# Kernel optimization log

Hardware: AMD Instinct MI355X
Metric: run time of the kernel (lower is better)

## Reference

```python
import jax, jax.numpy as jnp
import numpy as np

COMMITMENT_COST = 0.25
CODE_BOOK_SIZE = 1024
EMBED_DIM = 64


def setup_inputs() -> dict:
    key = jax.random.key(0)
    k1, k2 = jax.random.split(key)
    inputs = jax.random.normal(k1, (32, 64, 32, 32), dtype=jnp.float32)
    # matches torch init: uniform(-1/K, 1/K)
    embedding = jax.random.uniform(
        k2, (CODE_BOOK_SIZE, EMBED_DIM), dtype=jnp.float32,
        minval=-1.0 / CODE_BOOK_SIZE, maxval=1.0 / CODE_BOOK_SIZE)
    return {"inputs": inputs, "embedding": embedding}


def reference(inputs, embedding):
    # inputs: [B, D, H, W] -> [B, H, W, D]
    x = jnp.transpose(inputs, (0, 2, 3, 1))
    B, H, W, D = x.shape
    flat = x.reshape(-1, D)                                   # [N, D]
    # ((x - e)**2).mean(-1), without the [N, K, D] broadcast tensor)
    x2 = jnp.sum(flat * flat, axis=1, keepdims=True)          # [N, 1]
    e2 = jnp.sum(embedding * embedding, axis=1)               # [K]
    distances = (x2 - 2.0 * (flat @ embedding.T) + e2) / D    # [N, K]
    encoding_indices = jnp.argmin(distances, axis=1)          # [N]
    quantized = embedding[encoding_indices].reshape(B, H, W, D)
    e_latent_loss = jnp.mean((jax.lax.stop_gradient(quantized) - x) ** 2)
    q_latent_loss = jnp.mean((quantized - jax.lax.stop_gradient(x)) ** 2)
    loss = q_latent_loss + COMMITMENT_COST * e_latent_loss
    # straight-through estimator (training mode); value identical to quantized
    quantized = x + jax.lax.stop_gradient(quantized - x)
    return (loss,
            jnp.transpose(quantized, (0, 3, 1, 2)),
            encoding_indices.reshape(B, -1))
```

## Files before the change

### kernel.cpp

```cpp
#include <hip/hip_runtime.h>


constexpr int D_   = 64;
constexpr int HW   = 1024;
constexpr int K_   = 1024;
constexpr int PTS  = 128;
constexpr int SX   = 132;
constexpr int QE   = 2097152;
constexpr int IDX_OFF = 1 + QE;

__global__ __launch_bounds__(1024) void vq_main_kernel(
    const float* __restrict__ in, const float* __restrict__ emb,
    float* __restrict__ out, float* __restrict__ loss_acc,
    unsigned* __restrict__ cnt) {
  __shared__ float xT[D_ * SX];
  __shared__ float eT[4][D_ * 64];
  __shared__ float e2s[K_];
  __shared__ float x2s[PTS];
  __shared__ int   idx_sel[PTS];
  __shared__ float cmb_v[4][PTS];
  __shared__ int   cmb_i[4][PTS];
  __shared__ float redbuf[16];

  const int t   = threadIdx.x;
  const int g   = t >> 8;
  const int tg  = t & 255;
  const int tx  = tg & 15;
  const int ty  = tg >> 4;
  const int blk = blockIdx.x;
  const int b   = blk >> 3;
  const int hw0 = (blk & 7) * PTS;
  const float* inb = in + b * (D_ * HW) + hw0;

#pragma unroll
  for (int i = 0; i < 2; ++i) {
    int fi = t + i * 1024;
    int d  = fi >> 5, p4 = fi & 31;
    *(float4*)(&xT[d * SX + p4 * 4]) = *(const float4*)(inb + d * HW + p4 * 4);
  }

  {
    const float4* e4 = (const float4*)(emb + t * 64);
    float s = 0.f;
#pragma unroll
    for (int q = 0; q < 16; ++q) {
      float4 v = e4[q];
      s += v.x * v.x; s += v.y * v.y; s += v.z * v.z; s += v.w * v.w;
    }
    e2s[t] = s;
  }
  __syncthreads();

  if (t < PTS) {
    float s = 0.f;
#pragma unroll 8
    for (int d = 0; d < D_; ++d) { float xv = xT[d * SX + t]; s = fmaf(xv, xv, s); }
    x2s[t] = s;
  }
  __syncthreads();

  float x2r[8];
#pragma unroll
  for (int i = 0; i < 8; ++i) {
    int pi = (i < 4) ? ty * 4 + i : 64 + ty * 4 + (i - 4);
    x2r[i] = x2s[pi];
  }
  float minv[8]; int mini[8];
#pragma unroll
  for (int i = 0; i < 8; ++i) { minv[i] = 3.4e38f; mini[i] = 0; }

  for (int c = 0; c < 4; ++c) {
    const int kb = (g * 4 + c) * 64;
#pragma unroll
    for (int i = 0; i < 4; ++i) {
      int fi = tg + i * 256;
      int kl = fi >> 4, d4 = fi & 15;
      float4 v = *(const float4*)(emb + (kb + kl) * 64 + d4 * 4);
      int cpd = (((kl >> 2) ^ d4) << 2) | (kl & 3);
      float* eg = &eT[g][0];
      eg[(d4 * 4 + 0) * 64 + cpd] = v.x;
      eg[(d4 * 4 + 1) * 64 + cpd] = v.y;
      eg[(d4 * 4 + 2) * 64 + cpd] = v.z;
      eg[(d4 * 4 + 3) * 64 + cpd] = v.w;
    }
    __syncthreads();

    float acc[8][4];
#pragma unroll
    for (int i = 0; i < 8; ++i)
#pragma unroll
      for (int j = 0; j < 4; ++j) acc[i][j] = 0.f;

#pragma unroll 4
    for (int d = 0; d < D_; ++d) {
      float4 xa = *(const float4*)(&xT[d * SX + ty * 4]);
      float4 xb = *(const float4*)(&xT[d * SX + 64 + ty * 4]);
      float4 ea = *(const float4*)(&eT[g][d * 64 + ((tx ^ (d >> 2)) << 2)]);
      float xf[8] = {xa.x, xa.y, xa.z, xa.w, xb.x, xb.y, xb.z, xb.w};
      float ef[4] = {ea.x, ea.y, ea.z, ea.w};
#pragma unroll
      for (int i = 0; i < 8; ++i)
#pragma unroll
        for (int j = 0; j < 4; ++j)
          acc[i][j] = fmaf(xf[i], ef[j], acc[i][j]);
    }

#pragma unroll
    for (int j = 0; j < 4; ++j) {
      int cl = tx * 4 + j;
      float e2v = e2s[kb + cl];
      int cg = kb + cl;
#pragma unroll
      for (int i = 0; i < 8; ++i) {
        float u = fmaf(-2.f, acc[i][j], x2r[i]) + e2v;
        if (u < minv[i]) { minv[i] = u; mini[i] = cg; }
      }
    }
    __syncthreads();
  }

#pragma unroll
  for (int i = 0; i < 8; ++i) {
    float v = minv[i]; int ix = mini[i];
#pragma unroll
    for (int off = 1; off < 16; off <<= 1) {
      float vo = __shfl_xor(v, off);
      int   io = __shfl_xor(ix, off);
      if (vo < v || (vo == v && io < ix)) { v = vo; ix = io; }
    }
    if (tx == 0) {
      int pi = (i < 4) ? ty * 4 + i : 64 + ty * 4 + (i - 4);
      cmb_v[g][pi] = v; cmb_i[g][pi] = ix;
    }
  }
  __syncthreads();

  if (t < PTS) {
    float v = cmb_v[0][t]; int ix = cmb_i[0][t];
#pragma unroll
    for (int g2 = 1; g2 < 4; ++g2) {
      float vo = cmb_v[g2][t]; int io = cmb_i[g2][t];
      if (vo < v) { v = vo; ix = io; }
    }
    idx_sel[t] = ix;
    out[IDX_OFF + blk * PTS + t] = (float)ix;
  }
  __syncthreads();

  float lp = 0.f;
#pragma unroll
  for (int i = 0; i < 2; ++i) {
    int fi = t + i * 1024;
    int p = fi & 127, qd = fi >> 7;
    int cidx = idx_sel[p];
    float4 q = *(const float4*)(emb + cidx * 64 + qd * 4);
    float xv0 = xT[(qd * 4 + 0) * SX + p];
    float xv1 = xT[(qd * 4 + 1) * SX + p];
    float xv2 = xT[(qd * 4 + 2) * SX + p];
    float xv3 = xT[(qd * 4 + 3) * SX + p];
    float d0 = q.x - xv0, d1 = q.y - xv1, d2 = q.z - xv2, d3 = q.w - xv3;
    lp = fmaf(d0, d0, lp); lp = fmaf(d1, d1, lp);
    lp = fmaf(d2, d2, lp); lp = fmaf(d3, d3, lp);
    xT[(qd * 4 + 0) * SX + p] = xv0 + d0;
    xT[(qd * 4 + 1) * SX + p] = xv1 + d1;
    xT[(qd * 4 + 2) * SX + p] = xv2 + d2;
    xT[(qd * 4 + 3) * SX + p] = xv3 + d3;
  }

#pragma unroll
  for (int off = 1; off < 64; off <<= 1) lp += __shfl_xor(lp, off);
  if ((t & 63) == 0) redbuf[t >> 6] = lp;
  __syncthreads();
  if (t == 0) {
    float part = 0.f;
#pragma unroll
    for (int w = 0; w < 16; ++w) part += redbuf[w];
    atomicAdd(loss_acc, part);
    __threadfence();
    unsigned old = atomicAdd(cnt, 1u);
    if (old == 255u) {
      __threadfence();
      float total = atomicAdd(loss_acc, 0.0f);
      float m = total * (1.0f / 2097152.0f);
      out[0] = m + 0.25f * m;
    }
  }

  float* outq = out + 1 + b * (D_ * HW) + hw0;
#pragma unroll
  for (int i = 0; i < 8; ++i) {
    int oi = t + i * 1024;
    int d = oi >> 7, p = oi & 127;
    outq[d * HW + p] = xT[d * SX + p];
  }
}

extern "C" void kernel_launch(void* const* d_in, const int* in_sizes, int n_in,
                              void* d_out, int out_size, void* d_ws, size_t ws_size,
                              hipStream_t stream) {
  const float* in  = (const float*)d_in[0];
  const float* emb = (const float*)d_in[1];
  float* out = (float*)d_out;
  float* loss_acc = (float*)d_ws;
  unsigned* cnt   = (unsigned*)d_ws + 4;

  hipMemsetAsync(d_ws, 0, 64, stream);
  vq_main_kernel<<<256, 1024, 0, stream>>>(in, emb, out, loss_acc, cnt);
}
```

Before: 140.1 us.

## Retile VQ distance GEMM to 8x16 register tiles with staged codebook chunks

Restructures the kernel to 512 blocks of 256 threads covering 64 points each. Each thread now computes an 8-point by 16-code register tile, streaming the codebook through shared memory in 16-dim slices over two 512-code passes. This replaces the four-group split and its cross-group argmin merge with a single warp-level shuffle reduction. The goal is higher FMA-to-load ratio and better occupancy; the cost is heavy register pressure (128 accumulators) and more barriers per pass.

```diff
diff --git a/kernel.cpp b/kernel.cpp
--- a/kernel.cpp
+++ b/kernel.cpp
@@ -4,167 +4,183 @@
 constexpr int D_   = 64;
 constexpr int HW   = 1024;
 constexpr int K_   = 1024;
-constexpr int PTS  = 128;
-constexpr int SX   = 132;
+constexpr int PTS  = 64;
+constexpr int SP   = 68;
+constexpr int SEK  = 516;
 constexpr int QE   = 2097152;
 constexpr int IDX_OFF = 1 + QE;
 
-__global__ __launch_bounds__(1024) void vq_main_kernel(
+__global__ __launch_bounds__(256, 2) void vq_main_kernel(
     const float* __restrict__ in, const float* __restrict__ emb,
     float* __restrict__ out, float* __restrict__ loss_acc,
     unsigned* __restrict__ cnt) {
-  __shared__ float xT[D_ * SX];
-  __shared__ float eT[4][D_ * 64];
+  __shared__ float xT[D_ * SP];
+  __shared__ float eTs[16 * SEK];
   __shared__ float e2s[K_];
   __shared__ float x2s[PTS];
   __shared__ int   idx_sel[PTS];
-  __shared__ float cmb_v[4][PTS];
-  __shared__ int   cmb_i[4][PTS];
-  __shared__ float redbuf[16];
+  __shared__ float redbuf[4];
 
   const int t   = threadIdx.x;
-  const int g   = t >> 8;
-  const int tg  = t & 255;
-  const int tx  = tg & 15;
-  const int ty  = tg >> 4;
+  const int kg  = t & 31;
+  const int ptg = t >> 5;
   const int blk = blockIdx.x;
-  const int b   = blk >> 3;
-  const int hw0 = (blk & 7) * PTS;
+  const int b   = blk >> 4;
+  const int hw0 = (blk & 15) * PTS;
   const float* inb = in + b * (D_ * HW) + hw0;
 
 #pragma unroll
-  for (int i = 0; i < 2; ++i) {
-    int fi = t + i * 1024;
-    int d  = fi >> 5, p4 = fi & 31;
-    *(float4*)(&xT[d * SX + p4 * 4]) = *(const float4*)(inb + d * HW + p4 * 4);
-  }
-
-  {
-    const float4* e4 = (const float4*)(emb + t * 64);
+  for (int i = 0; i < 4; ++i) {
+    int fi = t + i * 256;
+    int d  = fi >> 4, p4 = fi & 15;
+    *(float4*)(&xT[d * SP + p4 * 4]) = *(const float4*)(inb + d * HW + p4 * 4);
+  }
+
+#pragma unroll
+  for (int c = 0; c < 4; ++c) {
+    int k = t + c * 256;
+    const float4* e4 = (const float4*)(emb + k * 64);
     float s = 0.f;
 #pragma unroll
     for (int q = 0; q < 16; ++q) {
       float4 v = e4[q];
       s += v.x * v.x; s += v.y * v.y; s += v.z * v.z; s += v.w * v.w;
     }
-    e2s[t] = s;
+    e2s[k] = s;
   }
   __syncthreads();
 
   if (t < PTS) {
     float s = 0.f;
 #pragma unroll 8
-    for (int d = 0; d < D_; ++d) { float xv = xT[d * SX + t]; s = fmaf(xv, xv, s); }
+    for (int d = 0; d < D_; ++d) { float xv = xT[d * SP + t]; s = fmaf(xv, xv, s); }
     x2s[t] = s;
   }
   __syncthreads();
 
   float x2r[8];
-#pragma unroll
-  for (int i = 0; i < 8; ++i) {
-    int pi = (i < 4) ? ty * 4 + i : 64 + ty * 4 + (i - 4);
-    x2r[i] = x2s[pi];
-  }
+  {
+    float4 xa = *(const float4*)&x2s[ptg * 8];
+    float4 xb = *(const float4*)&x2s[ptg * 8 + 4];
+    x2r[0]=xa.x; x2r[1]=xa.y; x2r[2]=xa.z; x2r[3]=xa.w;
+    x2r[4]=xb.x; x2r[5]=xb.y; x2r[6]=xb.z; x2r[7]=xb.w;
+  }
+
+  int eoff[4];
+#pragma unroll
+  for (int q = 0; q < 4; ++q)
+    eoff[q] = 4 * (((kg + q) & 7) + 8 * ((kg >> 3) + 4 * q));
+
   float minv[8]; int mini[8];
 #pragma unroll
   for (int i = 0; i < 8; ++i) { minv[i] = 3.4e38f; mini[i] = 0; }
 
-  for (int c = 0; c < 4; ++c) {
-    const int kb = (g * 4 + c) * 64;
-#pragma unroll
-    for (int i = 0; i < 4; ++i) {
-      int fi = tg + i * 256;
-      int kl = fi >> 4, d4 = fi & 15;
-      float4 v = *(const float4*)(emb + (kb + kl) * 64 + d4 * 4);
-      int cpd = (((kl >> 2) ^ d4) << 2) | (kl & 3);
-      float* eg = &eT[g][0];
-      eg[(d4 * 4 + 0) * 64 + cpd] = v.x;
-      eg[(d4 * 4 + 1) * 64 + cpd] = v.y;
-      eg[(d4 * 4 + 2) * 64 + cpd] = v.z;
-      eg[(d4 * 4 + 3) * 64 + cpd] = v.w;
-    }
-    __syncthreads();
-
-    float acc[8][4];
+#pragma unroll 1
+  for (int pass = 0; pass < 2; ++pass) {
+    float acc[8][16];
 #pragma unroll
     for (int i = 0; i < 8; ++i)
 #pragma unroll
-      for (int j = 0; j < 4; ++j) acc[i][j] = 0.f;
+      for (int j = 0; j < 16; ++j) acc[i][j] = 0.f;
+
+#pragma unroll 1
+    for (int s = 0; s < 4; ++s) {
+      __syncthreads();
+      {
+        int c0 = 2 * t;
+        int kgs = c0 >> 4, qs = (c0 >> 2) & 3, js = c0 & 3;
+        int Cc = 4 * (((kgs + qs) & 7) + 8 * ((kgs >> 3) + 4 * qs)) + js;
+        const float4* ga = (const float4*)(emb + (pass * 512 + c0) * 64 + s * 16);
+        const float4* gb = (const float4*)(emb + (pass * 512 + c0 + 1) * 64 + s * 16);
+        float4 a[4], bb[4];
+#pragma unroll
+        for (int r = 0; r < 4; ++r) { a[r] = ga[r]; bb[r] = gb[r]; }
+#pragma unroll
+        for (int r = 0; r < 4; ++r) {
+          float av[4] = {a[r].x, a[r].y, a[r].z, a[r].w};
+          float bv[4] = {bb[r].x, bb[r].y, bb[r].z, bb[r].w};
+#pragma unroll
+          for (int jd = 0; jd < 4; ++jd)
+            *(float2*)(&eTs[(r * 4 + jd) * SEK + Cc]) = make_float2(av[jd], bv[jd]);
+        }
+      }
+      __syncthreads();
 
 #pragma unroll 4
-    for (int d = 0; d < D_; ++d) {
-      float4 xa = *(const float4*)(&xT[d * SX + ty * 4]);
-      float4 xb = *(const float4*)(&xT[d * SX + 64 + ty * 4]);
-      float4 ea = *(const float4*)(&eT[g][d * 64 + ((tx ^ (d >> 2)) << 2)]);
-      float xf[8] = {xa.x, xa.y, xa.z, xa.w, xb.x, xb.y, xb.z, xb.w};
-      float ef[4] = {ea.x, ea.y, ea.z, ea.w};
-#pragma unroll
-      for (int i = 0; i < 8; ++i)
-#pragma unroll
-        for (int j = 0; j < 4; ++j)
-          acc[i][j] = fmaf(xf[i], ef[j], acc[i][j]);
-    }
-
-#pragma unroll
-    for (int j = 0; j < 4; ++j) {
-      int cl = tx * 4 + j;
-      float e2v = e2s[kb + cl];
-      int cg = kb + cl;
+      for (int dd = 0; dd < 16; ++dd) {
+        int drow = dd * SEK;
+        int dg   = s * 16 + dd;
+        float4 xa = *(const float4*)&xT[dg * SP + ptg * 8];
+        float4 xb = *(const float4*)&xT[dg * SP + ptg * 8 + 4];
+        float4 e0 = *(const float4*)&eTs[drow + eoff[0]];
+        float4 e1 = *(const float4*)&eTs[drow + eoff[1]];
+        float4 e2 = *(const float4*)&eTs[drow + eoff[2]];
+        float4 e3 = *(const float4*)&eTs[drow + eoff[3]];
+        float xf[8]  = {xa.x, xa.y, xa.z, xa.w, xb.x, xb.y, xb.z, xb.w};
+        float ef[16] = {e0.x, e0.y, e0.z, e0.w, e1.x, e1.y, e1.z, e1.w,
+                        e2.x, e2.y, e2.z, e2.w, e3.x, e3.y, e3.z, e3.w};
+#pragma unroll
+        for (int i = 0; i < 8; ++i)
+#pragma unroll
+          for (int j = 0; j < 16; ++j)
+            acc[i][j] = fmaf(xf[i], ef[j], acc[i][j]);
+      }
+    }
+
+    float e2f[16];
+    {
+      const float4* p4 = (const float4*)&e2s[pass * 512 + kg * 16];
+#pragma unroll
+      for (int q = 0; q < 4; ++q) {
+        float4 v = p4[q];
+        e2f[q*4+0]=v.x; e2f[q*4+1]=v.y; e2f[q*4+2]=v.z; e2f[q*4+3]=v.w;
+      }
+    }
+#pragma unroll
+    for (int j = 0; j < 16; ++j) {
+      int cg = pass * 512 + kg * 16 + j;
+      float e2v = e2f[j];
 #pragma unroll
       for (int i = 0; i < 8; ++i) {
         float u = fmaf(-2.f, acc[i][j], x2r[i]) + e2v;
         if (u < minv[i]) { minv[i] = u; mini[i] = cg; }
       }
     }
-    __syncthreads();
   }
 
 #pragma unroll
   for (int i = 0; i < 8; ++i) {
     float v = minv[i]; int ix = mini[i];
 #pragma unroll
-    for (int off = 1; off < 16; off <<= 1) {
+    for (int off = 1; off < 32; off <<= 1) {
       float vo = __shfl_xor(v, off);
       int   io = __shfl_xor(ix, off);
       if (vo < v || (vo == v && io < ix)) { v = vo; ix = io; }
     }
-    if (tx == 0) {
-      int pi = (i < 4) ? ty * 4 + i : 64 + ty * 4 + (i - 4);
-      cmb_v[g][pi] = v; cmb_i[g][pi] = ix;
-    }
-  }
-  __syncthreads();
-
-  if (t < PTS) {
-    float v = cmb_v[0][t]; int ix = cmb_i[0][t];
-#pragma unroll
-    for (int g2 = 1; g2 < 4; ++g2) {
-      float vo = cmb_v[g2][t]; int io = cmb_i[g2][t];
-      if (vo < v) { v = vo; ix = io; }
-    }
-    idx_sel[t] = ix;
-    out[IDX_OFF + blk * PTS + t] = (float)ix;
-  }
-  __syncthreads();
+    if (kg == 0) idx_sel[ptg * 8 + i] = ix;
+  }
+  __syncthreads();
+
+  if (t < PTS) out[IDX_OFF + blk * PTS + t] = (float)idx_sel[t];
 
   float lp = 0.f;
 #pragma unroll
-  for (int i = 0; i < 2; ++i) {
-    int fi = t + i * 1024;
-    int p = fi & 127, qd = fi >> 7;
+  for (int i = 0; i < 4; ++i) {
+    int fi = t + i * 256;
+    int p = fi & 63, qd = fi >> 6;
     int cidx = idx_sel[p];
     float4 q = *(const float4*)(emb + cidx * 64 + qd * 4);
-    float xv0 = xT[(qd * 4 + 0) * SX + p];
-    float xv1 = xT[(qd * 4 + 1) * SX + p];
-    float xv2 = xT[(qd * 4 + 2) * SX + p];
-    float xv3 = xT[(qd * 4 + 3) * SX + p];
+    float xv0 = xT[(qd * 4 + 0) * SP + p];
+    float xv1 = xT[(qd * 4 + 1) * SP + p];
+    float xv2 = xT[(qd * 4 + 2) * SP + p];
+    float xv3 = xT[(qd * 4 + 3) * SP + p];
     float d0 = q.x - xv0, d1 = q.y - xv1, d2 = q.z - xv2, d3 = q.w - xv3;
     lp = fmaf(d0, d0, lp); lp = fmaf(d1, d1, lp);
     lp = fmaf(d2, d2, lp); lp = fmaf(d3, d3, lp);
-    xT[(qd * 4 + 0) * SX + p] = xv0 + d0;
-    xT[(qd * 4 + 1) * SX + p] = xv1 + d1;
-    xT[(qd * 4 + 2) * SX + p] = xv2 + d2;
-    xT[(qd * 4 + 3) * SX + p] = xv3 + d3;
+    xT[(qd * 4 + 0) * SP + p] = xv0 + d0;
+    xT[(qd * 4 + 1) * SP + p] = xv1 + d1;
+    xT[(qd * 4 + 2) * SP + p] = xv2 + d2;
+    xT[(qd * 4 + 3) * SP + p] = xv3 + d3;
   }
 
 #pragma unroll
@@ -172,13 +188,10 @@
   if ((t & 63) == 0) redbuf[t >> 6] = lp;
   __syncthreads();
   if (t == 0) {
-    float part = 0.f;
-#pragma unroll
-    for (int w = 0; w < 16; ++w) part += redbuf[w];
-    atomicAdd(loss_acc, part);
+    atomicAdd(loss_acc, redbuf[0] + redbuf[1] + redbuf[2] + redbuf[3]);
     __threadfence();
     unsigned old = atomicAdd(cnt, 1u);
-    if (old == 255u) {
+    if (old == 511u) {
       __threadfence();
       float total = atomicAdd(loss_acc, 0.0f);
       float m = total * (1.0f / 2097152.0f);
@@ -188,10 +201,10 @@
 
   float* outq = out + 1 + b * (D_ * HW) + hw0;
 #pragma unroll
-  for (int i = 0; i < 8; ++i) {
-    int oi = t + i * 1024;
-    int d = oi >> 7, p = oi & 127;
-    outq[d * HW + p] = xT[d * SX + p];
+  for (int i = 0; i < 16; ++i) {
+    int oi = t + i * 256;
+    int d = oi >> 6, p = oi & 63;
+    outq[d * HW + p] = xT[d * SP + p];
   }
 }
 
@@ -205,5 +218,5 @@
   unsigned* cnt   = (unsigned*)d_ws + 4;
 
   hipMemsetAsync(d_ws, 0, 64, stream);
-  vq_main_kernel<<<256, 1024, 0, stream>>>(in, emb, out, loss_acc, cnt);
+  vq_main_kernel<<<512, 256, 0, stream>>>(in, emb, out, loss_acc, cnt);
 }
```

New measurement: 148.9 us. 1.06x slower.
